# Optimization experiments

Measured on AMD Instinct MI355X. Metric: run time of the kernel, lower is better.

Reference implementation:

```python
import jax, jax.numpy as jnp
import numpy as np

LN_EPS = 1e-5


def setup_inputs() -> dict:
    key = jax.random.key(0)
    ks = jax.random.split(key, 12)
    B, T, U, H, V = 4, 512, 128, 512, 41
    src = jax.random.normal(ks[0], (B, T, H), dtype=jnp.float32)
    tgt = jax.random.normal(ks[1], (B, U, H), dtype=jnp.float32)
    src_len = jax.random.randint(ks[2], (B,), 1, T + 1, dtype=jnp.int32)
    tgt_len = jax.random.randint(ks[3], (B,), 1, U + 1, dtype=jnp.int32)
    s = 1.0 / np.sqrt(H)
    W1 = jax.random.uniform(ks[4], (H, H), jnp.float32, -s, s)
    b1 = jax.random.uniform(ks[5], (H,), jnp.float32, -s, s)
    W2 = jax.random.uniform(ks[6], (H, H), jnp.float32, -s, s)
    b2 = jax.random.uniform(ks[7], (H,), jnp.float32, -s, s)
    ln_g = jnp.ones((H,), jnp.float32)
    ln_b = jnp.zeros((H,), jnp.float32)
    Wl = jax.random.uniform(ks[8], (H, V), jnp.float32, -s, s)
    bl = jax.random.uniform(ks[9], (V,), jnp.float32, -s, s)
    return dict(source_encodings=src, source_lengths=src_len,
                target_encodings=tgt, target_lengths=tgt_len,
                W1=W1, b1=b1, W2=W2, b2=b2, ln_g=ln_g, ln_b=ln_b,
                Wl=Wl, bl=bl)


def _f_target(tgt, W1, b1, W2, b2, ln_g, ln_b):
    h = jax.nn.gelu(tgt @ W1 + b1, approximate=False)  # exact GELU (torch default)
    h = h @ W2 + b2
    mu = jnp.mean(h, axis=-1, keepdims=True)
    var = jnp.var(h, axis=-1, keepdims=True)
    return (h - mu) * jax.lax.rsqrt(var + LN_EPS) * ln_g + ln_b


def reference(source_encodings, source_lengths, target_encodings, target_lengths,
              W1, b1, W2, b2, ln_g, ln_b, Wl, bl):
    tgt = _f_target(target_encodings, W1, b1, W2, b2, ln_g, ln_b)  # [B,U,H]
    # joint broadcast add: [B,T,1,H] + [B,1,U,H] -> [B,T,U,H]
    joint = source_encodings[:, :, None, :] + tgt[:, None, :, :]
    act = jnp.tanh(joint)
    out = act @ Wl + bl  # [B,T,U,V]
    return out, source_lengths, target_lengths
```

## Files before the change

### kernel.cpp

```cpp
#include <hip/hip_runtime.h>
#include <math.h>

#define Bb 4
#define Tt 512
#define Uu 128
#define Hh 512
#define Vv 41

typedef __attribute__((ext_vector_type(8))) short short8;
typedef __attribute__((ext_vector_type(4))) float f32x4;
typedef __attribute__((ext_vector_type(2))) float v2f;

__device__ __forceinline__ unsigned pack_bf16_rne(float hi, float lo) {
    unsigned xh = __float_as_uint(hi); xh += 0x7fffu + ((xh >> 16) & 1u);
    unsigned xl = __float_as_uint(lo); xl += 0x7fffu + ((xl >> 16) & 1u);
    return __builtin_amdgcn_perm(xh, xl, 0x07060302);
}

__device__ __forceinline__ unsigned tanh2_pack(v2f x) {
    v2f xc;
    xc.x = fminf(3.0f, fmaxf(-3.0f, x.x));
    xc.y = fminf(3.0f, fmaxf(-3.0f, x.y));
    v2f t = xc * xc;
    v2f p = t * (-0.00140725f) + 0.0288922f;
    p = p * t + (-0.2177528f);
    p = p * t + 0.9707868f;
    v2f g = xc * p;
    return __builtin_amdgcn_perm(__float_as_uint(g.y), __float_as_uint(g.x), 0x07060302);
}

__global__ __launch_bounds__(256) void prep_pack(
    const float* __restrict__ W1, const float* __restrict__ W2,
    const float* __restrict__ Wl,
    unsigned short* __restrict__ Wp1, unsigned short* __restrict__ Wp2,
    unsigned short* __restrict__ Wpl)
{
    __shared__ float T[64][65];
    const int bid = blockIdx.x, tid = threadIdx.x;
    const float* Wsrc; unsigned short* Wdst; int k0, n0, isWl;
    if (bid < 64)       { Wsrc = W1; Wdst = Wp1; k0 = (bid >> 3) * 64; n0 = (bid & 7) * 64; isWl = 0; }
    else if (bid < 128) { Wsrc = W2; Wdst = Wp2; k0 = ((bid - 64) >> 3) * 64; n0 = ((bid - 64) & 7) * 64; isWl = 0; }
    else                { Wsrc = Wl; Wdst = Wpl; k0 = (bid - 128) * 64; n0 = 0; isWl = 1; }

    #pragma unroll
    for (int i = 0; i < 16; ++i) {
        int idx = i * 256 + tid;
        int kk = idx >> 6, nn = idx & 63;
        float v;
        if (isWl) v = (nn < Vv) ? Wl[(k0 + kk) * Vv + nn] : 0.0f;
        else      v = Wsrc[(size_t)(k0 + kk) * 512 + n0 + nn];
        T[kk][nn] = v;
    }
    __syncthreads();

    #pragma unroll
    for (int i = 0; i < 2; ++i) {
        int task = i * 256 + tid;
        int nn = task & 63, kg = task >> 6;
        if (isWl && nn >= 48) continue;
        int n = n0 + nn, k = k0 + kg * 8;
        float e[8];
        #pragma unroll
        for (int j = 0; j < 8; ++j) e[j] = T[kg * 8 + j][nn];
        uint4 pk;
        pk.x = pack_bf16_rne(e[1], e[0]);
        pk.y = pack_bf16_rne(e[3], e[2]);
        pk.z = pack_bf16_rne(e[5], e[4]);
        pk.w = pack_bf16_rne(e[7], e[6]);
        int ntg = n >> 4, ncol = n & 15;
        int ks = (k >> 5) & 15, quad = (k >> 3) & 3;
        int lane = quad * 16 + ncol;
        *(uint4*)(Wdst + (size_t)((ntg * 16 + ks) * 64 + lane) * 8) = pk;
    }
}

__global__ __launch_bounds__(512) void target_kernel(
    const float* __restrict__ tgt,
    const unsigned short* __restrict__ Wp1, const float* __restrict__ b1,
    const unsigned short* __restrict__ Wp2, const float* __restrict__ b2,
    const float* __restrict__ ln_g, const float* __restrict__ ln_b,
    float* __restrict__ tgtPf)
{
    __shared__ unsigned short At[16][520];
    __shared__ float Ct[16][516];
    __shared__ float stats[16][2];

    const int tid = threadIdx.x;
    const int lane = tid & 63, wave = tid >> 6;
    const int ncol = lane & 15, quad = lane >> 4;
    const int r0 = blockIdx.x * 16;

    {
        const float4* t4 = (const float4*)(tgt + (size_t)r0 * Hh);
        #pragma unroll
        for (int j = 0; j < 4; ++j) {
            int fi = tid + j * 512;
            int row = fi >> 7, c4 = fi & 127;
            float4 v = t4[fi];
            uint2 pk;
            pk.x = pack_bf16_rne(v.y, v.x);
            pk.y = pack_bf16_rne(v.w, v.z);
            *(uint2*)&At[row][c4 * 4] = pk;
        }
    }
    __syncthreads();

    f32x4 acc[4];
    #pragma unroll
    for (int i = 0; i < 4; ++i) acc[i] = (f32x4){0.f, 0.f, 0.f, 0.f};

    const unsigned short* bp1 = Wp1 + (size_t)(wave * 4) * 8192 + lane * 8;
    const unsigned short* bp2 = Wp2 + (size_t)(wave * 4) * 8192 + lane * 8;

    #pragma unroll 2
    for (int ks = 0; ks < 16; ++ks) {
        int kb = ks * 32 + quad * 8;
        short8 af = *(const short8*)&At[ncol][kb];
        #pragma unroll
        for (int nt = 0; nt < 4; ++nt) {
            short8 bfr = *(const short8*)(bp1 + nt * 8192 + ks * 512);
            acc[nt] = __builtin_amdgcn_mfma_f32_16x16x32_bf16(af, bfr, acc[nt], 0, 0, 0);
        }
    }
    __syncthreads();

    #pragma unroll
    for (int nt = 0; nt < 4; ++nt) {
        int n = wave * 64 + nt * 16 + ncol;
        float bias = b1[n];
        #pragma unroll
        for (int r = 0; r < 4; ++r) {
            float v = acc[nt][r] + bias;
            float g = 0.5f * v * (1.0f + erff(v * 0.70710678118654752f));
            unsigned x = __float_as_uint(g); x += 0x7fffu + ((x >> 16) & 1u);
            At[quad * 4 + r][n] = (unsigned short)(x >> 16);
        }
        acc[nt] = (f32x4){0.f, 0.f, 0.f, 0.f};
    }
    __syncthreads();

    #pragma unroll 2
    for (int ks = 0; ks < 16; ++ks) {
        int kb = ks * 32 + quad * 8;
        short8 af = *(const short8*)&At[ncol][kb];
        #pragma unroll
        for (int nt = 0; nt < 4; ++nt) {
            short8 bfr = *(const short8*)(bp2 + nt * 8192 + ks * 512);
            acc[nt] = __builtin_amdgcn_mfma_f32_16x16x32_bf16(af, bfr, acc[nt], 0, 0, 0);
        }
    }

    #pragma unroll
    for (int nt = 0; nt < 4; ++nt) {
        int n = wave * 64 + nt * 16 + ncol;
        float bias = b2[n];
        #pragma unroll
        for (int r = 0; r < 4; ++r)
            Ct[quad * 4 + r][n] = acc[nt][r] + bias;
    }
    __syncthreads();

    const int row = tid >> 5, l32 = tid & 31;
    const float4* cr = (const float4*)&Ct[row][0];
    float s = 0.f, q = 0.f;
    #pragma unroll
    for (int j = 0; j < 4; ++j) {
        float4 v = cr[l32 + 32 * j];
        s += v.x + v.y + v.z + v.w;
        q += v.x * v.x + v.y * v.y + v.z * v.z + v.w * v.w;
    }
    #pragma unroll
    for (int off = 16; off > 0; off >>= 1) {
        s += __shfl_down(s, off, 32);
        q += __shfl_down(q, off, 32);
    }
    if (l32 == 0) {
        float mu = s * (1.0f / Hh);
        float var = q * (1.0f / Hh) - mu * mu;
        stats[row][0] = mu;
        stats[row][1] = rsqrtf(var + 1e-5f);
    }
    __syncthreads();
    {
        float mu = stats[row][0], rs = stats[row][1];
        int r = r0 + row;
        int bb = r >> 7, u = r & 127;
        float* obase = tgtPf + (size_t)bb * 65536 + u * 8;
        #pragma unroll
        for (int j = 0; j < 4; ++j) {
            int c4 = l32 + 32 * j;
            float4 v = cr[c4];
            float4 g4 = ((const float4*)ln_g)[c4];
            float4 b4 = ((const float4*)ln_b)[c4];
            float4 o;
            o.x = (v.x - mu) * rs * g4.x + b4.x;
            o.y = (v.y - mu) * rs * g4.y + b4.y;
            o.z = (v.z - mu) * rs * g4.z + b4.z;
            o.w = (v.w - mu) * rs * g4.w + b4.w;
            *(float4*)(obase + (c4 >> 1) * 1024 + (c4 & 1) * 4) = o;
        }
    }
}

__global__ __launch_bounds__(256) void joint_mfma(
    const float* __restrict__ src, const float* __restrict__ tgtPf,
    const unsigned short* __restrict__ Wpl, const float* __restrict__ bl,
    float* __restrict__ out)
{
    __shared__ float srcl[2 * Hh];

    const int t0 = blockIdx.x * 2, b = blockIdx.y, uh = blockIdx.z;
    const int tid = threadIdx.x;
    const int lane = tid & 63, wave = tid >> 6;
    const int ncol = lane & 15, quad = lane >> 4;

    const float4* s4 = (const float4*)(src + ((size_t)(b * Tt + t0)) * Hh);
    ((float4*)srcl)[tid] = s4[tid];

    float bln[3];
    #pragma unroll
    for (int nt = 0; nt < 3; ++nt) {
        int n = nt * 16 + ncol;
        bln[nt] = (n < Vv) ? bl[n] : 0.0f;
    }

    f32x4 acc[2][3];
    #pragma unroll
    for (int mi = 0; mi < 2; ++mi)
        #pragma unroll
        for (int nt = 0; nt < 3; ++nt)
            acc[mi][nt] = (f32x4){0.f, 0.f, 0.f, 0.f};

    __syncthreads();

    const int u0 = uh * 64 + (wave & 1) * 32 + ncol;
    const float* pA = tgtPf + (size_t)b * 65536 + u0 * 8;
    const float* srow = srcl + (wave >> 1) * Hh;
    const unsigned short* bp = Wpl + lane * 8;

    #pragma unroll 2
    for (int ks = 0; ks < 16; ++ks) {
        const int off = (ks * 4 + quad) * 1024;
        float4 a0 = *(const float4*)(pA + off);
        float4 a1 = *(const float4*)(pA + off + 4);
        float4 c0 = *(const float4*)(pA + off + 128);
        float4 c1 = *(const float4*)(pA + off + 132);
        const float* sp = srow + ks * 32 + quad * 8;
        float4 sA = *(const float4*)(sp);
        float4 sB = *(const float4*)(sp + 4);

        union { uint4 u; short8 s; } f0, f1;
        f0.u.x = tanh2_pack((v2f){sA.x + a0.x, sA.y + a0.y});
        f0.u.y = tanh2_pack((v2f){sA.z + a0.z, sA.w + a0.w});
        f0.u.z = tanh2_pack((v2f){sB.x + a1.x, sB.y + a1.y});
        f0.u.w = tanh2_pack((v2f){sB.z + a1.z, sB.w + a1.w});
        f1.u.x = tanh2_pack((v2f){sA.x + c0.x, sA.y + c0.y});
        f1.u.y = tanh2_pack((v2f){sA.z + c0.z, sA.w + c0.w});
        f1.u.z = tanh2_pack((v2f){sB.x + c1.x, sB.y + c1.y});
        f1.u.w = tanh2_pack((v2f){sB.z + c1.z, sB.w + c1.w});

        #pragma unroll
        for (int nt = 0; nt < 3; ++nt) {
            short8 bfr = *(const short8*)(bp + (nt * 16 + ks) * 512);
            acc[0][nt] = __builtin_amdgcn_mfma_f32_16x16x32_bf16(f0.s, bfr, acc[0][nt], 0, 0, 0);
            acc[1][nt] = __builtin_amdgcn_mfma_f32_16x16x32_bf16(f1.s, bfr, acc[1][nt], 0, 0, 0);
        }
    }

    const int t = t0 + (wave >> 1);
    const int ub = uh * 64 + (wave & 1) * 32;
    float* ob = out + ((size_t)(b * Tt + t)) * Uu * Vv;
    #pragma unroll
    for (int mi = 0; mi < 2; ++mi) {
        #pragma unroll
        for (int nt = 0; nt < 3; ++nt) {
            int n = nt * 16 + ncol;
            if (n < Vv) {
                #pragma unroll
                for (int r = 0; r < 4; ++r) {
                    int m = ub + mi * 16 + quad * 4 + r;
                    ob[m * Vv + n] = acc[mi][nt][r] + bln[nt];
                }
            }
        }
    }
}

__global__ void len_kernel(const int* __restrict__ sl, const int* __restrict__ tl,
                           float* __restrict__ dst)
{
    const int i = threadIdx.x;
    if (i < Bb)            dst[i] = (float)sl[i];
    else if (i < 2 * Bb)   dst[i] = (float)tl[i - Bb];
}

extern "C" void kernel_launch(void* const* d_in, const int* in_sizes, int n_in,
                              void* d_out, int out_size, void* d_ws, size_t ws_size,
                              hipStream_t stream)
{
    const float* src  = (const float*)d_in[0];
    const int*   slen = (const int*)  d_in[1];
    const float* tgt  = (const float*)d_in[2];
    const int*   tlen = (const int*)  d_in[3];
    const float* W1   = (const float*)d_in[4];
    const float* b1   = (const float*)d_in[5];
    const float* W2   = (const float*)d_in[6];
    const float* b2   = (const float*)d_in[7];
    const float* ln_g = (const float*)d_in[8];
    const float* ln_b = (const float*)d_in[9];
    const float* Wl   = (const float*)d_in[10];
    const float* bl   = (const float*)d_in[11];

    float* out = (float*)d_out;
    float* tgtPf = (float*)d_ws;
    unsigned short* Wp1 = (unsigned short*)((char*)d_ws + 1048576);
    unsigned short* Wp2 = (unsigned short*)((char*)d_ws + 1048576 + 524288);
    unsigned short* Wpl = (unsigned short*)((char*)d_ws + 2097152);

    hipLaunchKernelGGL(prep_pack, dim3(136), dim3(256), 0, stream,
                       W1, W2, Wl, Wp1, Wp2, Wpl);
    hipLaunchKernelGGL(target_kernel, dim3(Bb * Uu / 16), dim3(512), 0, stream,
                       tgt, Wp1, b1, Wp2, b2, ln_g, ln_b, tgtPf);
    hipLaunchKernelGGL(joint_mfma, dim3(Tt / 2, Bb, 2), dim3(256), 0, stream,
                       src, tgtPf, Wpl, bl, out);
    hipLaunchKernelGGL(len_kernel, dim3(1), dim3(64), 0, stream,
                       slen, tlen, out + (size_t)Bb * Tt * Uu * Vv);
}
```

Before: 150.1 us.

## Prefetch operands in joint and target GEMMs, widen target blocks, fold length kernel

The joint kernel now loads the next k-step's target operands one iteration ahead in registers, and the loop unroll goes from 2 to 4. The target kernel moves to 1024 threads with two N-tiles per wave and register-prefetched B fragments. LayerNorm is now done one row per wave with xor shuffles, which removes a shared-memory stats pass and a barrier. The length-conversion kernel is folded into prep_pack to save one launch, and the tanh clamp uses fmed3. The prefetching raises register pressure, which could lower occupancy in the dominant joint kernel.

```diff
diff --git a/kernel.cpp b/kernel.cpp
--- a/kernel.cpp
+++ b/kernel.cpp
@@ -17,14 +17,20 @@
     return __builtin_amdgcn_perm(xh, xl, 0x07060302);
 }
 
-__device__ __forceinline__ unsigned tanh2_pack(v2f x) {
+__device__ __forceinline__ unsigned short bf16_rne(float v) {
+    unsigned x = __float_as_uint(v);
+    x += 0x7fffu + ((x >> 16) & 1u);
+    return (unsigned short)(x >> 16);
+}
+
+__device__ __forceinline__ unsigned tanh2_pack(float x0, float x1) {
     v2f xc;
-    xc.x = fminf(3.0f, fmaxf(-3.0f, x.x));
-    xc.y = fminf(3.0f, fmaxf(-3.0f, x.y));
+    xc.x = __builtin_amdgcn_fmed3f(x0, -3.0f, 3.0f);
+    xc.y = __builtin_amdgcn_fmed3f(x1, -3.0f, 3.0f);
     v2f t = xc * xc;
-    v2f p = t * (-0.00140725f) + 0.0288922f;
-    p = p * t + (-0.2177528f);
-    p = p * t + 0.9707868f;
+    v2f p = t * (v2f){-0.00140725f, -0.00140725f} + (v2f){0.0288922f, 0.0288922f};
+    p = p * t + (v2f){-0.2177528f, -0.2177528f};
+    p = p * t + (v2f){0.9707868f, 0.9707868f};
     v2f g = xc * p;
     return __builtin_amdgcn_perm(__float_as_uint(g.y), __float_as_uint(g.x), 0x07060302);
 }
@@ -33,10 +39,17 @@
     const float* __restrict__ W1, const float* __restrict__ W2,
     const float* __restrict__ Wl,
     unsigned short* __restrict__ Wp1, unsigned short* __restrict__ Wp2,
-    unsigned short* __restrict__ Wpl)
+    unsigned short* __restrict__ Wpl,
+    const int* __restrict__ sl, const int* __restrict__ tl,
+    float* __restrict__ lenDst)
 {
     __shared__ float T[64][65];
     const int bid = blockIdx.x, tid = threadIdx.x;
+
+    if (bid == 135 && tid < 2 * Bb) {
+        lenDst[tid] = (tid < Bb) ? (float)sl[tid] : (float)tl[tid - Bb];
+    }
+
     const float* Wsrc; unsigned short* Wdst; int k0, n0, isWl;
     if (bid < 64)       { Wsrc = W1; Wdst = Wp1; k0 = (bid >> 3) * 64; n0 = (bid & 7) * 64; isWl = 0; }
     else if (bid < 128) { Wsrc = W2; Wdst = Wp2; k0 = ((bid - 64) >> 3) * 64; n0 = ((bid - 64) & 7) * 64; isWl = 0; }
@@ -74,7 +87,7 @@
     }
 }
 
-__global__ __launch_bounds__(512) void target_kernel(
+__global__ __launch_bounds__(1024) void target_kernel(
     const float* __restrict__ tgt,
     const unsigned short* __restrict__ Wp1, const float* __restrict__ b1,
     const unsigned short* __restrict__ Wp2, const float* __restrict__ b2,
@@ -83,7 +96,6 @@
 {
     __shared__ unsigned short At[16][520];
     __shared__ float Ct[16][516];
-    __shared__ float stats[16][2];
 
     const int tid = threadIdx.x;
     const int lane = tid & 63, wave = tid >> 6;
@@ -93,8 +105,8 @@
     {
         const float4* t4 = (const float4*)(tgt + (size_t)r0 * Hh);
         #pragma unroll
-        for (int j = 0; j < 4; ++j) {
-            int fi = tid + j * 512;
+        for (int j = 0; j < 2; ++j) {
+            int fi = tid + j * 1024;
             int row = fi >> 7, c4 = fi & 127;
             float4 v = t4[fi];
             uint2 pk;
@@ -105,54 +117,65 @@
     }
     __syncthreads();
 
-    f32x4 acc[4];
-    #pragma unroll
-    for (int i = 0; i < 4; ++i) acc[i] = (f32x4){0.f, 0.f, 0.f, 0.f};
-
-    const unsigned short* bp1 = Wp1 + (size_t)(wave * 4) * 8192 + lane * 8;
-    const unsigned short* bp2 = Wp2 + (size_t)(wave * 4) * 8192 + lane * 8;
-
-    #pragma unroll 2
-    for (int ks = 0; ks < 16; ++ks) {
-        int kb = ks * 32 + quad * 8;
-        short8 af = *(const short8*)&At[ncol][kb];
-        #pragma unroll
-        for (int nt = 0; nt < 4; ++nt) {
-            short8 bfr = *(const short8*)(bp1 + nt * 8192 + ks * 512);
-            acc[nt] = __builtin_amdgcn_mfma_f32_16x16x32_bf16(af, bfr, acc[nt], 0, 0, 0);
-        }
-    }
-    __syncthreads();
-
-    #pragma unroll
-    for (int nt = 0; nt < 4; ++nt) {
-        int n = wave * 64 + nt * 16 + ncol;
+    f32x4 acc[2];
+    acc[0] = (f32x4){0.f, 0.f, 0.f, 0.f};
+    acc[1] = (f32x4){0.f, 0.f, 0.f, 0.f};
+
+    const unsigned short* bp1 = Wp1 + (size_t)(wave * 2) * 8192 + lane * 8;
+    const unsigned short* bp2 = Wp2 + (size_t)(wave * 2) * 8192 + lane * 8;
+
+    {
+        short8 cb0 = *(const short8*)(bp1);
+        short8 cb1 = *(const short8*)(bp1 + 8192);
+        #pragma unroll
+        for (int ks = 0; ks < 16; ++ks) {
+            short8 nb0, nb1;
+            if (ks < 15) {
+                nb0 = *(const short8*)(bp1 + (ks + 1) * 512);
+                nb1 = *(const short8*)(bp1 + 8192 + (ks + 1) * 512);
+            }
+            short8 af = *(const short8*)&At[ncol][ks * 32 + quad * 8];
+            acc[0] = __builtin_amdgcn_mfma_f32_16x16x32_bf16(af, cb0, acc[0], 0, 0, 0);
+            acc[1] = __builtin_amdgcn_mfma_f32_16x16x32_bf16(af, cb1, acc[1], 0, 0, 0);
+            cb0 = nb0; cb1 = nb1;
+        }
+    }
+    __syncthreads();
+
+    #pragma unroll
+    for (int nt = 0; nt < 2; ++nt) {
+        int n = wave * 32 + nt * 16 + ncol;
         float bias = b1[n];
         #pragma unroll
         for (int r = 0; r < 4; ++r) {
             float v = acc[nt][r] + bias;
             float g = 0.5f * v * (1.0f + erff(v * 0.70710678118654752f));
-            unsigned x = __float_as_uint(g); x += 0x7fffu + ((x >> 16) & 1u);
-            At[quad * 4 + r][n] = (unsigned short)(x >> 16);
+            At[quad * 4 + r][n] = bf16_rne(g);
         }
         acc[nt] = (f32x4){0.f, 0.f, 0.f, 0.f};
     }
     __syncthreads();
 
-    #pragma unroll 2
-    for (int ks = 0; ks < 16; ++ks) {
-        int kb = ks * 32 + quad * 8;
-        short8 af = *(const short8*)&At[ncol][kb];
-        #pragma unroll
-        for (int nt = 0; nt < 4; ++nt) {
-            short8 bfr = *(const short8*)(bp2 + nt * 8192 + ks * 512);
-            acc[nt] = __builtin_amdgcn_mfma_f32_16x16x32_bf16(af, bfr, acc[nt], 0, 0, 0);
-        }
-    }
-
-    #pragma unroll
-    for (int nt = 0; nt < 4; ++nt) {
-        int n = wave * 64 + nt * 16 + ncol;
+    {
+        short8 cb0 = *(const short8*)(bp2);
+        short8 cb1 = *(const short8*)(bp2 + 8192);
+        #pragma unroll
+        for (int ks = 0; ks < 16; ++ks) {
+            short8 nb0, nb1;
+            if (ks < 15) {
+                nb0 = *(const short8*)(bp2 + (ks + 1) * 512);
+                nb1 = *(const short8*)(bp2 + 8192 + (ks + 1) * 512);
+            }
+            short8 af = *(const short8*)&At[ncol][ks * 32 + quad * 8];
+            acc[0] = __builtin_amdgcn_mfma_f32_16x16x32_bf16(af, cb0, acc[0], 0, 0, 0);
+            acc[1] = __builtin_amdgcn_mfma_f32_16x16x32_bf16(af, cb1, acc[1], 0, 0, 0);
+            cb0 = nb0; cb1 = nb1;
+        }
+    }
+
+    #pragma unroll
+    for (int nt = 0; nt < 2; ++nt) {
+        int n = wave * 32 + nt * 16 + ncol;
         float bias = b2[n];
         #pragma unroll
         for (int r = 0; r < 4; ++r)
@@ -160,44 +183,38 @@
     }
     __syncthreads();
 
-    const int row = tid >> 5, l32 = tid & 31;
-    const float4* cr = (const float4*)&Ct[row][0];
-    float s = 0.f, q = 0.f;
-    #pragma unroll
-    for (int j = 0; j < 4; ++j) {
-        float4 v = cr[l32 + 32 * j];
-        s += v.x + v.y + v.z + v.w;
-        q += v.x * v.x + v.y * v.y + v.z * v.z + v.w * v.w;
-    }
-    #pragma unroll
-    for (int off = 16; off > 0; off >>= 1) {
-        s += __shfl_down(s, off, 32);
-        q += __shfl_down(q, off, 32);
-    }
-    if (l32 == 0) {
+    {
+        const int row = wave;
+        const float2* cr2 = (const float2*)&Ct[row][0];
+        float2 vv[4];
+        float s = 0.f, q = 0.f;
+        #pragma unroll
+        for (int j = 0; j < 4; ++j) {
+            float2 v = cr2[lane + 64 * j];
+            vv[j] = v;
+            s += v.x + v.y;
+            q += v.x * v.x + v.y * v.y;
+        }
+        #pragma unroll
+        for (int off = 32; off > 0; off >>= 1) {
+            s += __shfl_xor(s, off, 64);
+            q += __shfl_xor(q, off, 64);
+        }
         float mu = s * (1.0f / Hh);
-        float var = q * (1.0f / Hh) - mu * mu;
-        stats[row][0] = mu;
-        stats[row][1] = rsqrtf(var + 1e-5f);
-    }
-    __syncthreads();
-    {
-        float mu = stats[row][0], rs = stats[row][1];
+        float rs = rsqrtf(q * (1.0f / Hh) - mu * mu + 1e-5f);
         int r = r0 + row;
         int bb = r >> 7, u = r & 127;
         float* obase = tgtPf + (size_t)bb * 65536 + u * 8;
         #pragma unroll
         for (int j = 0; j < 4; ++j) {
-            int c4 = l32 + 32 * j;
-            float4 v = cr[c4];
-            float4 g4 = ((const float4*)ln_g)[c4];
-            float4 b4 = ((const float4*)ln_b)[c4];
-            float4 o;
-            o.x = (v.x - mu) * rs * g4.x + b4.x;
-            o.y = (v.y - mu) * rs * g4.y + b4.y;
-            o.z = (v.z - mu) * rs * g4.z + b4.z;
-            o.w = (v.w - mu) * rs * g4.w + b4.w;
-            *(float4*)(obase + (c4 >> 1) * 1024 + (c4 & 1) * 4) = o;
+            int k2 = lane + 64 * j;
+            int k = k2 * 2;
+            float2 g2 = ((const float2*)ln_g)[k2];
+            float2 bv = ((const float2*)ln_b)[k2];
+            float2 o;
+            o.x = (vv[j].x - mu) * rs * g2.x + bv.x;
+            o.y = (vv[j].y - mu) * rs * g2.y + bv.y;
+            *(float2*)(obase + ((k >> 3) << 10) + (k & 7)) = o;
         }
     }
 }
@@ -217,6 +234,15 @@
     const float4* s4 = (const float4*)(src + ((size_t)(b * Tt + t0)) * Hh);
     ((float4*)srcl)[tid] = s4[tid];
 
+    const int u0 = uh * 64 + (wave & 1) * 32 + ncol;
+    const float* pA = tgtPf + (size_t)b * 65536 + u0 * 8;
+    const unsigned short* bp = Wpl + lane * 8;
+
+    float4 a0 = *(const float4*)(pA + quad * 1024);
+    float4 a1 = *(const float4*)(pA + quad * 1024 + 4);
+    float4 c0 = *(const float4*)(pA + quad * 1024 + 128);
+    float4 c1 = *(const float4*)(pA + quad * 1024 + 132);
+
     float bln[3];
     #pragma unroll
     for (int nt = 0; nt < 3; ++nt) {
@@ -233,31 +259,31 @@
 
     __syncthreads();
 
-    const int u0 = uh * 64 + (wave & 1) * 32 + ncol;
-    const float* pA = tgtPf + (size_t)b * 65536 + u0 * 8;
     const float* srow = srcl + (wave >> 1) * Hh;
-    const unsigned short* bp = Wpl + lane * 8;
-
-    #pragma unroll 2
+
+    #pragma unroll 4
     for (int ks = 0; ks < 16; ++ks) {
-        const int off = (ks * 4 + quad) * 1024;
-        float4 a0 = *(const float4*)(pA + off);
-        float4 a1 = *(const float4*)(pA + off + 4);
-        float4 c0 = *(const float4*)(pA + off + 128);
-        float4 c1 = *(const float4*)(pA + off + 132);
+        float4 na0, na1, nc0, nc1;
+        if (ks < 15) {
+            const float* pn = pA + ((ks + 1) * 4 + quad) * 1024;
+            na0 = *(const float4*)(pn);
+            na1 = *(const float4*)(pn + 4);
+            nc0 = *(const float4*)(pn + 128);
+            nc1 = *(const float4*)(pn + 132);
+        }
         const float* sp = srow + ks * 32 + quad * 8;
         float4 sA = *(const float4*)(sp);
         float4 sB = *(const float4*)(sp + 4);
 
         union { uint4 u; short8 s; } f0, f1;
-        f0.u.x = tanh2_pack((v2f){sA.x + a0.x, sA.y + a0.y});
-        f0.u.y = tanh2_pack((v2f){sA.z + a0.z, sA.w + a0.w});
-        f0.u.z = tanh2_pack((v2f){sB.x + a1.x, sB.y + a1.y});
-        f0.u.w = tanh2_pack((v2f){sB.z + a1.z, sB.w + a1.w});
-        f1.u.x = tanh2_pack((v2f){sA.x + c0.x, sA.y + c0.y});
-        f1.u.y = tanh2_pack((v2f){sA.z + c0.z, sA.w + c0.w});
-        f1.u.z = tanh2_pack((v2f){sB.x + c1.x, sB.y + c1.y});
-        f1.u.w = tanh2_pack((v2f){sB.z + c1.z, sB.w + c1.w});
+        f0.u.x = tanh2_pack(sA.x + a0.x, sA.y + a0.y);
+        f0.u.y = tanh2_pack(sA.z + a0.z, sA.w + a0.w);
+        f0.u.z = tanh2_pack(sB.x + a1.x, sB.y + a1.y);
+        f0.u.w = tanh2_pack(sB.z + a1.z, sB.w + a1.w);
+        f1.u.x = tanh2_pack(sA.x + c0.x, sA.y + c0.y);
+        f1.u.y = tanh2_pack(sA.z + c0.z, sA.w + c0.w);
+        f1.u.z = tanh2_pack(sB.x + c1.x, sB.y + c1.y);
+        f1.u.w = tanh2_pack(sB.z + c1.z, sB.w + c1.w);
 
         #pragma unroll
         for (int nt = 0; nt < 3; ++nt) {
@@ -265,6 +291,7 @@
             acc[0][nt] = __builtin_amdgcn_mfma_f32_16x16x32_bf16(f0.s, bfr, acc[0][nt], 0, 0, 0);
             acc[1][nt] = __builtin_amdgcn_mfma_f32_16x16x32_bf16(f1.s, bfr, acc[1][nt], 0, 0, 0);
         }
+        a0 = na0; a1 = na1; c0 = nc0; c1 = nc1;
     }
 
     const int t = t0 + (wave >> 1);
@@ -284,14 +311,6 @@
             }
         }
     }
-}
-
-__global__ void len_kernel(const int* __restrict__ sl, const int* __restrict__ tl,
-                           float* __restrict__ dst)
-{
-    const int i = threadIdx.x;
-    if (i < Bb)            dst[i] = (float)sl[i];
-    else if (i < 2 * Bb)   dst[i] = (float)tl[i - Bb];
 }
 
 extern "C" void kernel_launch(void* const* d_in, const int* in_sizes, int n_in,
@@ -318,11 +337,10 @@
     unsigned short* Wpl = (unsigned short*)((char*)d_ws + 2097152);
 
     hipLaunchKernelGGL(prep_pack, dim3(136), dim3(256), 0, stream,
-                       W1, W2, Wl, Wp1, Wp2, Wpl);
-    hipLaunchKernelGGL(target_kernel, dim3(Bb * Uu / 16), dim3(512), 0, stream,
+                       W1, W2, Wl, Wp1, Wp2, Wpl,
+                       slen, tlen, out + (size_t)Bb * Tt * Uu * Vv);
+    hipLaunchKernelGGL(target_kernel, dim3(Bb * Uu / 16), dim3(1024), 0, stream,
                        tgt, Wp1, b1, Wp2, b2, ln_g, ln_b, tgtPf);
     hipLaunchKernelGGL(joint_mfma, dim3(Tt / 2, Bb, 2), dim3(256), 0, stream,
                        src, tgtPf, Wpl, bl, out);
-    hipLaunchKernelGGL(len_kernel, dim3(1), dim3(64), 0, stream,
-                       slen, tlen, out + (size_t)Bb * Tt * Uu * Vv);
-}
+}
```

Result: faster. 144.4 us (-3.8%).
